# Kernel tuning notes

Measured on AMD Instinct MI355X. Metric: run time of the kernel, lower is better.

Reference implementation:

```python
import jax, jax.numpy as jnp
import numpy as np

N_WORDS = 30000
EMB_DIM = 784          # must be a perfect square
MAT_DIM = 28           # sqrt(784)
BATCH = 256
SEQ_LEN = 64


def setup_inputs() -> dict:
    key = jax.random.key(0)
    k_sent, k_w = jax.random.split(key)
    # token ids in [1, N_WORDS]; row 0 of the table is the identity (neutral) element
    sent = jax.random.randint(k_sent, (BATCH, SEQ_LEN), 1, N_WORDS + 1, dtype=jnp.int64) \
        if jax.config.jax_enable_x64 else \
        jax.random.randint(k_sent, (BATCH, SEQ_LEN), 1, N_WORDS + 1, dtype=jnp.int32)
    # 'identity' initialization: N(0, 0.1) + flattened identity, prepended identity neutral row
    eye_flat = jnp.eye(MAT_DIM, dtype=jnp.float32).reshape(-1)        # [784]
    init_w = 0.1 * jax.random.normal(k_w, (N_WORDS, EMB_DIM), dtype=jnp.float32) + eye_flat
    lookup_weight = jnp.concatenate([eye_flat[None, :], init_w], axis=0)  # [N_WORDS+1, 784]
    return {"sent": sent, "lookup_weight": lookup_weight}


def reference(sent, lookup_weight):
    # CMOW: embedding lookup, reshape each word vector to a 28x28 matrix,
    # then a left-to-right chain of matrix products over the sequence.
    B, S = sent.shape
    mats = lookup_weight[sent].reshape(B, S, MAT_DIM, MAT_DIM)   # [B, S, 28, 28]
    # Log-depth parallel prefix product over the sequence axis (matmul is associative).
    prods = jax.lax.associative_scan(lambda a, b: a @ b, mats, axis=1)
    cur_emb = prods[:, -1]                                       # [B, 28, 28]
    return cur_emb.reshape(-1, EMB_DIM)                          # [B, 784]
```

## Files before the change

### kernel.cpp

```cpp
#include <hip/hip_runtime.h>
#include <hip/hip_bf16.h>


typedef float f32x2  __attribute__((ext_vector_type(2)));
typedef float f32x4  __attribute__((ext_vector_type(4)));
typedef float f32x16 __attribute__((ext_vector_type(16)));
typedef short bf16x8 __attribute__((ext_vector_type(8)));

namespace {
constexpr int MD  = 28;
constexpr int EMB = 784;
constexpr int SEQ = 64;
constexpr int BATCH = 256;
constexpr int SEG = 8;
constexpr int LEN = 8;
constexpr int LDP = 34;
}

__device__ __forceinline__ bf16x8 mkfrag(uint32_t w0, uint32_t w1,
                                         uint32_t w2, uint32_t w3) {
  union { uint32_t w[4]; bf16x8 b; } u;
  u.w[0] = w0; u.w[1] = w1; u.w[2] = w2; u.w[3] = w3;
  return u.b;
}

__device__ __forceinline__ void split8(const float* x, bf16x8& hi, bf16x8& lo) {
  uint32_t H[4], L[4];
#pragma unroll
  for (int p = 0; p < 4; ++p) {
    float x0 = x[2 * p], x1 = x[2 * p + 1];
    uint32_t h0 = __float_as_uint(x0) & 0xffff0000u;
    uint32_t h1 = __float_as_uint(x1) & 0xffff0000u;
    float l0 = x0 - __uint_as_float(h0);
    float l1 = x1 - __uint_as_float(h1);
    H[p] = (h0 >> 16) | h1;
    L[p] = (__float_as_uint(l0) >> 16) | (__float_as_uint(l1) & 0xffff0000u);
  }
  hi = mkfrag(H[0], H[1], H[2], H[3]);
  lo = mkfrag(L[0], L[1], L[2], L[3]);
}

__global__ __launch_bounds__(64)
__attribute__((amdgpu_waves_per_eu(2, 2)))
void w2m_partial_mfma(const int* __restrict__ sent,
                      const float* __restrict__ W,
                      float* __restrict__ ws) {
  __shared__ __align__(16) float Ms[2][EMB];
  __shared__ __align__(16) float RL[32][LDP];

  const int blk   = blockIdx.x;
  const int batch = blk >> 3;
  const int seg   = blk & 7;
  const int lane  = threadIdx.x;
  const int n = lane & 31;
  const int h = lane >> 5;
  const int* srow = sent + batch * SEQ + seg * LEN;

  f32x4 st0, st1, st2, st3;
  auto gstage = [&](int t) {
    const f32x4* src = reinterpret_cast<const f32x4*>(W + (size_t)srow[t] * EMB);
    st0 = src[lane];
    st1 = src[64 + lane];
    st2 = src[128 + lane];
    if (lane < 4) st3 = src[192 + lane];
  };
  auto lpublish = [&](int buf) {
    f32x4* d_ = reinterpret_cast<f32x4*>(Ms[buf]);
    d_[lane] = st0;
    d_[64 + lane] = st1;
    d_[128 + lane] = st2;
    if (lane < 4) d_[192 + lane] = st3;
  };

  float a[16];
  {
    const float* __restrict__ M0 = W + (size_t)srow[0] * EMB;
    const int m = n;
#pragma unroll
    for (int K = 0; K < 2; ++K)
#pragma unroll
      for (int u = 0; u < 2; ++u) {
        int k0 = 16 * K + 8 * h + 4 * u;
        f32x4 v = {0.f, 0.f, 0.f, 0.f};
        if (m < MD && k0 < MD)
          v = *reinterpret_cast<const f32x4*>(M0 + m * MD + k0);
        a[K * 8 + 4 * u + 0] = v[0];
        a[K * 8 + 4 * u + 1] = v[1];
        a[K * 8 + 4 * u + 2] = v[2];
        a[K * 8 + 4 * u + 3] = v[3];
      }
  }

  gstage(1);
  lpublish(1);
  gstage(2);

  f32x16 d;
#pragma unroll
  for (int t = 1; t < LEN; ++t) {
    const float* __restrict__ Mt = Ms[t & 1];
    float bb[16];
#pragma unroll
    for (int K = 0; K < 2; ++K)
#pragma unroll
      for (int e = 0; e < 8; ++e) {
        int k = 16 * K + 8 * h + e;
        int km = k < MD ? k : 0;
        int nm = n < MD ? n : 0;
        float v = Mt[km * MD + nm];
        bb[K * 8 + e] = (k < MD && n < MD) ? v : 0.f;
      }

    bf16x8 ah0, al0, ah1, al1, bh0, bl0, bh1, bl1;
    split8(a,      ah0, al0);
    split8(a + 8,  ah1, al1);
    split8(bb,     bh0, bl0);
    split8(bb + 8, bh1, bl1);

#pragma unroll
    for (int q = 0; q < 16; ++q) d[q] = 0.f;
    d = __builtin_amdgcn_mfma_f32_32x32x16_bf16(ah0, bh0, d, 0, 0, 0);
    d = __builtin_amdgcn_mfma_f32_32x32x16_bf16(ah0, bl0, d, 0, 0, 0);
    d = __builtin_amdgcn_mfma_f32_32x32x16_bf16(al0, bh0, d, 0, 0, 0);
    d = __builtin_amdgcn_mfma_f32_32x32x16_bf16(ah1, bh1, d, 0, 0, 0);
    d = __builtin_amdgcn_mfma_f32_32x32x16_bf16(ah1, bl1, d, 0, 0, 0);
    d = __builtin_amdgcn_mfma_f32_32x32x16_bf16(al1, bh1, d, 0, 0, 0);

    if (t < LEN - 1) {
      lpublish((t + 1) & 1);
      if (t + 2 < LEN) gstage(t + 2);

#pragma unroll
      for (int e = 0; e < 16; ++e) {
        int r = (e & 3) + 8 * (e >> 2) + 4 * h;
        RL[r][n] = d[e];
      }
      const int m = n;
#pragma unroll
      for (int K = 0; K < 2; ++K)
#pragma unroll
        for (int u = 0; u < 4; ++u) {
          int k0 = 16 * K + 8 * h + 2 * u;
          f32x2 v = *reinterpret_cast<const f32x2*>(&RL[m][k0]);
          a[K * 8 + 2 * u + 0] = v[0];
          a[K * 8 + 2 * u + 1] = v[1];
        }
    }
  }

  float* pb = ws + (size_t)(batch * SEG + seg) * EMB;
  if (n < MD) {
    if ((seg & 1) == 0) {
#pragma unroll
      for (int q = 0; q < 4; ++q) {
        int rbase = 8 * q + 4 * h;
        if (rbase < MD) {
          f32x4 v = { d[4 * q], d[4 * q + 1], d[4 * q + 2], d[4 * q + 3] };
          *reinterpret_cast<f32x4*>(pb + n * MD + rbase) = v;
        }
      }
    } else {
#pragma unroll
      for (int e = 0; e < 16; ++e) {
        int r = (e & 3) + 8 * (e >> 2) + 4 * h;
        if (r < MD) pb[r * MD + n] = d[e];
      }
    }
  }
}


__device__ __forceinline__ void kloop(const float* __restrict__ A,
                                      const float* __restrict__ B,
                                      int r0, int c0,
                                      f32x4& a0, f32x4& a1, f32x4& a2, f32x4& a3) {
  f32x4 z = {0.f, 0.f, 0.f, 0.f};
  a0 = a1 = a2 = a3 = z;
#pragma unroll
  for (int k = 0; k < MD; ++k) {
    f32x4 rv = *reinterpret_cast<const f32x4*>(A + k * MD + r0);
    f32x4 mv = *reinterpret_cast<const f32x4*>(B + k * MD + c0);
    a0 += rv[0] * mv;
    a1 += rv[1] * mv;
    a2 += rv[2] * mv;
    a3 += rv[3] * mv;
  }
}

__device__ __forceinline__ void store_T(float* __restrict__ D, int r0, int c0,
                                        const f32x4& a0, const f32x4& a1,
                                        const f32x4& a2, const f32x4& a3) {
#pragma unroll
  for (int cc = 0; cc < 4; ++cc) {
    f32x4 v = { a0[cc], a1[cc], a2[cc], a3[cc] };
    *reinterpret_cast<f32x4*>(D + (c0 + cc) * MD + r0) = v;
  }
}

__device__ __forceinline__ void store_N(float* __restrict__ D, int r0, int c0,
                                        const f32x4& a0, const f32x4& a1,
                                        const f32x4& a2, const f32x4& a3) {
  *reinterpret_cast<f32x4*>(D + (r0 + 0) * MD + c0) = a0;
  *reinterpret_cast<f32x4*>(D + (r0 + 1) * MD + c0) = a1;
  *reinterpret_cast<f32x4*>(D + (r0 + 2) * MD + c0) = a2;
  *reinterpret_cast<f32x4*>(D + (r0 + 3) * MD + c0) = a3;
}

__global__ __launch_bounds__(256, 1)
void w2m_combine(const float* __restrict__ ws, float* __restrict__ out) {
  __shared__ __align__(16) float P[SEG][EMB];
  __shared__ __align__(16) float Q[4][EMB];
  __shared__ __align__(16) float Rl[2][EMB];

  const int batch = blockIdx.x;
  const int tid   = threadIdx.x;
  const int w     = tid >> 6;
  const int lane  = tid & 63;
  const bool act  = lane < 49;
  const int i = lane / 7, j = lane % 7;
  const int r0 = 4 * i, c0 = 4 * j;

  {
    const f32x4* src = reinterpret_cast<const f32x4*>(ws + (size_t)batch * SEG * EMB);
    f32x4* dst = reinterpret_cast<f32x4*>(&P[0][0]);
    for (int u = tid; u < SEG * EMB / 4; u += 256) dst[u] = src[u];
  }
  __syncthreads();

  f32x4 a0, a1, a2, a3;
  if (act) {
    kloop(P[2 * w], P[2 * w + 1], r0, c0, a0, a1, a2, a3);
    if (w & 1) store_N(Q[w], r0, c0, a0, a1, a2, a3);
    else       store_T(Q[w], r0, c0, a0, a1, a2, a3);
  }
  __syncthreads();
  if (w < 2 && act) {
    kloop(Q[2 * w], Q[2 * w + 1], r0, c0, a0, a1, a2, a3);
    if (w & 1) store_N(Rl[w], r0, c0, a0, a1, a2, a3);
    else       store_T(Rl[w], r0, c0, a0, a1, a2, a3);
  }
  __syncthreads();
  if (w == 0 && act) {
    kloop(Rl[0], Rl[1], r0, c0, a0, a1, a2, a3);
    store_N(out + (size_t)batch * EMB, r0, c0, a0, a1, a2, a3);
  }
}

extern "C" void kernel_launch(void* const* d_in, const int* in_sizes, int n_in,
                              void* d_out, int out_size, void* d_ws, size_t ws_size,
                              hipStream_t stream) {
  const int*   sent = (const int*)d_in[0];
  const float* W    = (const float*)d_in[1];
  float*       out  = (float*)d_out;
  float*       ws   = (float*)d_ws;
  (void)in_sizes; (void)n_in; (void)out_size; (void)ws_size;

  w2m_partial_mfma<<<BATCH * SEG, 64, 0, stream>>>(sent, W, ws);
  w2m_combine<<<BATCH, 256, 0, stream>>>(ws, out);
}
```

Baseline: 139.2 us.

## Split sequence into 16 segments of 4 and add a combine tree level

The partial kernel now gives each batch 16 blocks of 4 words each instead of 8 blocks of 8. This shortens each block's serial MFMA chain and doubles the number of blocks. The combine kernel grows to 512 threads and gains one more pairwise reduction level to fold 16 partial products. The partial kernel also drops its double-buffered LDS for a single zero-padded buffer, which removes the bounds masking on the B-fragment loads, and uses an odd RL row pitch with scalar reads. In exchange, more workspace traffic passes through the combine kernel, and the combine tree gets longer with a larger LDS footprint.

```diff
diff --git a/kernel.cpp b/kernel.cpp
--- a/kernel.cpp
+++ b/kernel.cpp
@@ -2,7 +2,6 @@
 #include <hip/hip_bf16.h>
 
 
-typedef float f32x2  __attribute__((ext_vector_type(2)));
 typedef float f32x4  __attribute__((ext_vector_type(4)));
 typedef float f32x16 __attribute__((ext_vector_type(16)));
 typedef short bf16x8 __attribute__((ext_vector_type(8)));
@@ -12,9 +11,9 @@
 constexpr int EMB = 784;
 constexpr int SEQ = 64;
 constexpr int BATCH = 256;
-constexpr int SEG = 8;
-constexpr int LEN = 8;
-constexpr int LDP = 34;
+constexpr int SEG = 16;
+constexpr int LEN = 4;
+constexpr int RLP = 33;
 }
 
 __device__ __forceinline__ bf16x8 mkfrag(uint32_t w0, uint32_t w1,
@@ -41,20 +40,23 @@
 }
 
 __global__ __launch_bounds__(64)
-__attribute__((amdgpu_waves_per_eu(2, 2)))
+__attribute__((amdgpu_waves_per_eu(3, 4)))
 void w2m_partial_mfma(const int* __restrict__ sent,
                       const float* __restrict__ W,
                       float* __restrict__ ws) {
-  __shared__ __align__(16) float Ms[2][EMB];
-  __shared__ __align__(16) float RL[32][LDP];
+  __shared__ __align__(16) float Ms[1024];
+  __shared__ __align__(16) float RL[32 * RLP];
 
   const int blk   = blockIdx.x;
-  const int batch = blk >> 3;
-  const int seg   = blk & 7;
+  const int batch = blk >> 4;
+  const int seg   = blk & 15;
   const int lane  = threadIdx.x;
   const int n = lane & 31;
   const int h = lane >> 5;
   const int* srow = sent + batch * SEQ + seg * LEN;
+
+  if (lane < 60) *reinterpret_cast<f32x4*>(&Ms[784 + 4 * lane]) =
+      (f32x4){0.f, 0.f, 0.f, 0.f};
 
   f32x4 st0, st1, st2, st3;
   auto gstage = [&](int t) {
@@ -64,8 +66,8 @@
     st2 = src[128 + lane];
     if (lane < 4) st3 = src[192 + lane];
   };
-  auto lpublish = [&](int buf) {
-    f32x4* d_ = reinterpret_cast<f32x4*>(Ms[buf]);
+  auto lpublish = [&]() {
+    f32x4* d_ = reinterpret_cast<f32x4*>(Ms);
     d_[lane] = st0;
     d_[64 + lane] = st1;
     d_[128 + lane] = st2;
@@ -92,23 +94,19 @@
   }
 
   gstage(1);
-  lpublish(1);
+  lpublish();
   gstage(2);
 
   f32x16 d;
 #pragma unroll
   for (int t = 1; t < LEN; ++t) {
-    const float* __restrict__ Mt = Ms[t & 1];
     float bb[16];
 #pragma unroll
     for (int K = 0; K < 2; ++K)
 #pragma unroll
       for (int e = 0; e < 8; ++e) {
         int k = 16 * K + 8 * h + e;
-        int km = k < MD ? k : 0;
-        int nm = n < MD ? n : 0;
-        float v = Mt[km * MD + nm];
-        bb[K * 8 + e] = (k < MD && n < MD) ? v : 0.f;
+        bb[K * 8 + e] = Ms[k * MD + n];
       }
 
     bf16x8 ah0, al0, ah1, al1, bh0, bl0, bh1, bl1;
@@ -127,23 +125,21 @@
     d = __builtin_amdgcn_mfma_f32_32x32x16_bf16(al1, bh1, d, 0, 0, 0);
 
     if (t < LEN - 1) {
-      lpublish((t + 1) & 1);
+      lpublish();
       if (t + 2 < LEN) gstage(t + 2);
 
 #pragma unroll
       for (int e = 0; e < 16; ++e) {
         int r = (e & 3) + 8 * (e >> 2) + 4 * h;
-        RL[r][n] = d[e];
+        RL[r * RLP + n] = d[e];
       }
       const int m = n;
 #pragma unroll
       for (int K = 0; K < 2; ++K)
 #pragma unroll
-        for (int u = 0; u < 4; ++u) {
-          int k0 = 16 * K + 8 * h + 2 * u;
-          f32x2 v = *reinterpret_cast<const f32x2*>(&RL[m][k0]);
-          a[K * 8 + 2 * u + 0] = v[0];
-          a[K * 8 + 2 * u + 1] = v[1];
+        for (int e = 0; e < 8; ++e) {
+          int k = 16 * K + 8 * h + e;
+          a[K * 8 + e] = RL[m * RLP + k];
         }
     }
   }
@@ -206,11 +202,12 @@
   *reinterpret_cast<f32x4*>(D + (r0 + 3) * MD + c0) = a3;
 }
 
-__global__ __launch_bounds__(256, 1)
+__global__ __launch_bounds__(512, 1)
 void w2m_combine(const float* __restrict__ ws, float* __restrict__ out) {
   __shared__ __align__(16) float P[SEG][EMB];
-  __shared__ __align__(16) float Q[4][EMB];
-  __shared__ __align__(16) float Rl[2][EMB];
+  __shared__ __align__(16) float Q8[8][EMB];
+  __shared__ __align__(16) float Q4[4][EMB];
+  __shared__ __align__(16) float Q2[2][EMB];
 
   const int batch = blockIdx.x;
   const int tid   = threadIdx.x;
@@ -223,25 +220,31 @@
   {
     const f32x4* src = reinterpret_cast<const f32x4*>(ws + (size_t)batch * SEG * EMB);
     f32x4* dst = reinterpret_cast<f32x4*>(&P[0][0]);
-    for (int u = tid; u < SEG * EMB / 4; u += 256) dst[u] = src[u];
+    for (int u = tid; u < SEG * EMB / 4; u += 512) dst[u] = src[u];
   }
   __syncthreads();
 
   f32x4 a0, a1, a2, a3;
   if (act) {
     kloop(P[2 * w], P[2 * w + 1], r0, c0, a0, a1, a2, a3);
-    if (w & 1) store_N(Q[w], r0, c0, a0, a1, a2, a3);
-    else       store_T(Q[w], r0, c0, a0, a1, a2, a3);
+    if (w & 1) store_N(Q8[w], r0, c0, a0, a1, a2, a3);
+    else       store_T(Q8[w], r0, c0, a0, a1, a2, a3);
+  }
+  __syncthreads();
+  if (w < 4 && act) {
+    kloop(Q8[2 * w], Q8[2 * w + 1], r0, c0, a0, a1, a2, a3);
+    if (w & 1) store_N(Q4[w], r0, c0, a0, a1, a2, a3);
+    else       store_T(Q4[w], r0, c0, a0, a1, a2, a3);
   }
   __syncthreads();
   if (w < 2 && act) {
-    kloop(Q[2 * w], Q[2 * w + 1], r0, c0, a0, a1, a2, a3);
-    if (w & 1) store_N(Rl[w], r0, c0, a0, a1, a2, a3);
-    else       store_T(Rl[w], r0, c0, a0, a1, a2, a3);
+    kloop(Q4[2 * w], Q4[2 * w + 1], r0, c0, a0, a1, a2, a3);
+    if (w & 1) store_N(Q2[w], r0, c0, a0, a1, a2, a3);
+    else       store_T(Q2[w], r0, c0, a0, a1, a2, a3);
   }
   __syncthreads();
   if (w == 0 && act) {
-    kloop(Rl[0], Rl[1], r0, c0, a0, a1, a2, a3);
+    kloop(Q2[0], Q2[1], r0, c0, a0, a1, a2, a3);
     store_N(out + (size_t)batch * EMB, r0, c0, a0, a1, a2, a3);
   }
 }
@@ -256,5 +259,5 @@
   (void)in_sizes; (void)n_in; (void)out_size; (void)ws_size;
 
   w2m_partial_mfma<<<BATCH * SEG, 64, 0, stream>>>(sent, W, ws);
-  w2m_combine<<<BATCH, 256, 0, stream>>>(ws, out);
-}
+  w2m_combine<<<BATCH, 512, 0, stream>>>(ws, out);
+}
```

Measured after the change: 141.1 us. About the same (+1.4%).
